# Kernel tuning notes

Measured on AMD Instinct MI355X. Metric: run time of the kernel, lower is better.

The kernel has to match this reference:

```python
import jax, jax.numpy as jnp
import numpy as np

N_NODES = 50000
N_HEDGES = 10000
NNZ_INC = 400000
NNZ_E = 80000
NNZ_V = 400000
VDIM = 128
EDIM = 128
OUT_VDIM = 128
OUT_EDIM = 128


def _spmm(rows, cols, vals, X, n_rows):
    # sparse COO [n_rows, n_cols] @ X  -> [n_rows, d]
    return jax.ops.segment_sum(vals[:, None] * X[cols], rows, num_segments=n_rows)


def setup_inputs() -> dict:
    key = jax.random.key(0)
    ks = jax.random.split(key, 20)
    inp = {
        "vfeat": jax.random.normal(ks[0], (N_NODES, VDIM), jnp.float32),
        "efeat": jax.random.normal(ks[1], (N_HEDGES, EDIM), jnp.float32),
        "invDV": jax.random.uniform(ks[2], (N_NODES,), jnp.float32),
        "invDE": jax.random.uniform(ks[3], (N_HEDGES,), jnp.float32),
        "inc_src": jax.random.randint(ks[4], (NNZ_INC,), 0, N_NODES, jnp.int32),
        "inc_dst": jax.random.randint(ks[5], (NNZ_INC,), 0, N_HEDGES, jnp.int32),
        "emat_rows": jax.random.randint(ks[6], (NNZ_E,), 0, N_HEDGES, jnp.int32),
        "emat_cols": jax.random.randint(ks[7], (NNZ_E,), 0, N_HEDGES, jnp.int32),
        "emat_vals": jax.random.normal(ks[8], (NNZ_E,), jnp.float32),
        "vmat_rows": jax.random.randint(ks[9], (NNZ_V,), 0, N_NODES, jnp.int32),
        "vmat_cols": jax.random.randint(ks[10], (NNZ_V,), 0, N_NODES, jnp.int32),
        "vmat_vals": jax.random.normal(ks[11], (NNZ_V,), jnp.float32),
        # parameters (torch Linear: y = x @ W.T + b)
        "Wv": jax.random.normal(ks[12], (OUT_VDIM, VDIM), jnp.float32) * 0.05,
        "We": jax.random.normal(ks[13], (OUT_EDIM, EDIM), jnp.float32) * 0.05,
        "psi1_W": jax.random.normal(ks[14], (VDIM, VDIM + EDIM), jnp.float32) * 0.05,
        "psi1_b": jnp.zeros((VDIM,), jnp.float32),
        "psi2_W": jax.random.normal(ks[15], (EDIM, OUT_VDIM + EDIM), jnp.float32) * 0.05,
        "psi2_b": jnp.zeros((EDIM,), jnp.float32),
    }
    return inp


def reference(vfeat, efeat, invDV, invDE, inc_src, inc_dst,
              emat_rows, emat_cols, emat_vals,
              vmat_rows, vmat_cols, vmat_vals,
              Wv, We, psi1_W, psi1_b, psi2_W, psi2_b):
    N = vfeat.shape[0]
    E = efeat.shape[0]
    # --- 'in' update_all with psi1: per-incidence concat -> linear -> *invDV[src] -> sum into hyperedge
    x = jnp.concatenate([vfeat[inc_src], efeat[inc_dst]], axis=1)  # [nnz, VDIM+EDIM]
    x = x @ psi1_W.T + psi1_b                                       # [nnz, VDIM]
    x = x * invDV[inc_src][:, None]
    A = jax.ops.segment_sum(x, inc_dst, num_segments=E)             # [E, VDIM]
    A = _spmm(emat_rows, emat_cols, emat_vals, A, E)
    _efeat = A + efeat
    # --- 'con' update_all: node gathers sum of incident hyperedge feats
    _vfeat = jax.ops.segment_sum(_efeat[inc_dst], inc_src, num_segments=N)
    vfeat_out = jax.nn.relu(_vfeat @ Wv.T)                           # [N, OUT_VDIM]
    # --- 'in' update_all with psi2 (dv = ones)
    x2 = jnp.concatenate([vfeat_out[inc_src], efeat[inc_dst]], axis=1)
    x2 = x2 @ psi2_W.T + psi2_b                                      # [nnz, EDIM]
    B = jax.ops.segment_sum(x2, inc_dst, num_segments=E) * invDE[:, None]
    # --- 'con' pass with efeat, then vMat spmm, then 'in' sum back to hyperedges
    _vfeat2 = jax.ops.segment_sum(efeat[inc_dst], inc_src, num_segments=N)
    _vfeat2 = _spmm(vmat_rows, vmat_cols, vmat_vals, _vfeat2, N)
    _efeat2 = jax.ops.segment_sum(_vfeat2[inc_src], inc_dst, num_segments=E)
    _efeat2 = _efeat2 + B
    efeat_out = jax.nn.relu(_efeat2 @ We.T)                          # [E, OUT_EDIM]
    return vfeat_out, efeat_out
```

## Files before the change

kernel.cpp:

```cpp
#include <hip/hip_runtime.h>

#define NN 50000
#define NE 10000
#define NNZ_INC 400000
#define NNZ_E 80000
#define NNZ_V 400000
#define D 128
#define KC 32

#define CAP_D 112
#define CAP_S 40
#define CAP_E 40
#define CAP_V 40

#define GN_ 782
#define GE_ 157
#define G_HINC ((NNZ_INC + 255) / 256)
#define G_EV ((NNZ_E + NNZ_V + 255) / 256)
#define G_CVTN 6250
#define G_CVTE 1250
#define G_NR16 (NN / 16)
#define G_ER16 (NE / 16)

typedef unsigned short u16;
typedef unsigned int u32;

__device__ __forceinline__ u16 f2bf(float x) {
    unsigned u = __float_as_uint(x);
    unsigned r = u + 0x7fffu + ((u >> 16) & 1u);
    return (u16)(r >> 16);
}
__device__ __forceinline__ float bf2f(u16 h) {
    return __uint_as_float(((unsigned)h) << 16);
}

__device__ __forceinline__ void acc8(uint4 u, float acc[8]) {
    acc[0] += __uint_as_float(u.x << 16);
    acc[1] += __uint_as_float(u.x & 0xffff0000u);
    acc[2] += __uint_as_float(u.y << 16);
    acc[3] += __uint_as_float(u.y & 0xffff0000u);
    acc[4] += __uint_as_float(u.z << 16);
    acc[5] += __uint_as_float(u.z & 0xffff0000u);
    acc[6] += __uint_as_float(u.w << 16);
    acc[7] += __uint_as_float(u.w & 0xffff0000u);
}
__device__ __forceinline__ void fma8(uint4 u, float v, float acc[8]) {
    acc[0] = fmaf(v, __uint_as_float(u.x << 16), acc[0]);
    acc[1] = fmaf(v, __uint_as_float(u.x & 0xffff0000u), acc[1]);
    acc[2] = fmaf(v, __uint_as_float(u.y << 16), acc[2]);
    acc[3] = fmaf(v, __uint_as_float(u.y & 0xffff0000u), acc[3]);
    acc[4] = fmaf(v, __uint_as_float(u.z << 16), acc[4]);
    acc[5] = fmaf(v, __uint_as_float(u.z & 0xffff0000u), acc[5]);
    acc[6] = fmaf(v, __uint_as_float(u.w << 16), acc[6]);
    acc[7] = fmaf(v, __uint_as_float(u.w & 0xffff0000u), acc[7]);
}
__device__ __forceinline__ uint4 pack_bf8(const float acc[8]) {
    uint4 o;
    o.x = (u32)f2bf(acc[0]) | ((u32)f2bf(acc[1]) << 16);
    o.y = (u32)f2bf(acc[2]) | ((u32)f2bf(acc[3]) << 16);
    o.z = (u32)f2bf(acc[4]) | ((u32)f2bf(acc[5]) << 16);
    o.w = (u32)f2bf(acc[6]) | ((u32)f2bf(acc[7]) << 16);
    return o;
}

__device__ __forceinline__ void gemm_acc(
    int bx, const float* __restrict__ X, const float* __restrict__ W, int ldw,
    int M, float acc[8][4])
{
    __shared__ float XsT[KC][68];
    __shared__ float Ws[KC][132];
    const int tid = threadIdx.x;
    const int tx = tid & 31, ty = tid >> 5;
    const int row0 = bx * 64;
    const int c0 = tx * 4;
    const int r0 = ty * 8;

#pragma unroll
    for (int r = 0; r < 8; ++r)
#pragma unroll
        for (int c = 0; c < 4; ++c) acc[r][c] = 0.f;

    for (int kc = 0; kc < D; kc += KC) {
        __syncthreads();
#pragma unroll
        for (int it = 0; it < 2; ++it) {
            int l = tid + it * 256;
            int r = l >> 3, k4 = l & 7;
            float4 v = make_float4(0.f, 0.f, 0.f, 0.f);
            int row = row0 + r;
            if (row < M) v = ((const float4*)(X + (size_t)row * D + kc))[k4];
            int k = k4 * 4;
            XsT[k + 0][r] = v.x; XsT[k + 1][r] = v.y;
            XsT[k + 2][r] = v.z; XsT[k + 3][r] = v.w;
        }
#pragma unroll
        for (int it = 0; it < 4; ++it) {
            int l = tid + it * 256;
            int o = l >> 3, k4 = l & 7;
            float4 w = ((const float4*)(W + (size_t)o * ldw + kc))[k4];
            int k = k4 * 4;
            Ws[k + 0][o] = w.x; Ws[k + 1][o] = w.y;
            Ws[k + 2][o] = w.z; Ws[k + 3][o] = w.w;
        }
        __syncthreads();
#pragma unroll
        for (int k = 0; k < KC; ++k) {
            const float4 a0 = *(const float4*)&XsT[k][r0];
            const float4 a1 = *(const float4*)&XsT[k][r0 + 4];
            const float4 b  = *(const float4*)&Ws[k][c0];
            float av[8] = {a0.x, a0.y, a0.z, a0.w, a1.x, a1.y, a1.z, a1.w};
            float bv[4] = {b.x, b.y, b.z, b.w};
#pragma unroll
            for (int r = 0; r < 8; ++r)
#pragma unroll
                for (int c = 0; c < 4; ++c)
                    acc[r][c] = fmaf(av[r], bv[c], acc[r][c]);
        }
    }
}

__global__ __launch_bounds__(256) void mega0(
    const int* __restrict__ inc_src, const int* __restrict__ inc_dst,
    int* __restrict__ cnt_dst, int* __restrict__ cnt_src,
    u16* __restrict__ ell_d, u16* __restrict__ ell_s,
    const float* __restrict__ efeat, const float* __restrict__ vfeat,
    const float* __restrict__ invDV,
    u16* __restrict__ vfi_b, u16* __restrict__ efeat_b)
{
    int b = blockIdx.x;
    if (b < G_HINC) {
        int i = b * 256 + threadIdx.x;
        if (i < NNZ_INC) {
            int s = inc_src[i], d = inc_dst[i];
            int rd = atomicAdd(cnt_dst + d, 1);
            if (rd < CAP_D) ell_d[d * CAP_D + rd] = (u16)s;
            int rs = atomicAdd(cnt_src + s, 1);
            if (rs < CAP_S) ell_s[s * CAP_S + rs] = (u16)d;
        }
    } else if (b < G_HINC + G_CVTN) {
        int i = ((b - G_HINC) * 256 + threadIdx.x) * 4;
        int row = i >> 7;
        float s = invDV[row];
        float4 v = *(const float4*)(vfeat + i);
        ushort4 u;
        u.x = f2bf(v.x * s); u.y = f2bf(v.y * s);
        u.z = f2bf(v.z * s); u.w = f2bf(v.w * s);
        *(ushort4*)(vfi_b + i) = u;
    } else {
        int i = ((b - G_HINC - G_CVTN) * 256 + threadIdx.x) * 4;
        float4 v = *(const float4*)(efeat + i);
        ushort4 u;
        u.x = f2bf(v.x); u.y = f2bf(v.y); u.z = f2bf(v.z); u.w = f2bf(v.w);
        *(ushort4*)(efeat_b + i) = u;
    }
}

__device__ __forceinline__ void segsum_bf_ell16(int rb,
    const int* __restrict__ cnt, int cap, const u16* __restrict__ ell,
    const u16* __restrict__ Tb, u16* __restrict__ Yb, int R)
{
    int r = rb * 16 + (threadIdx.x >> 4);
    int q = threadIdx.x & 15;
    if (r >= R) return;
    int m = min(cnt[r], cap);
    const u16* lst = ell + (size_t)r * cap;
    float acc[8] = {0.f, 0.f, 0.f, 0.f, 0.f, 0.f, 0.f, 0.f};
    int j = 0;
    for (; j + 3 < m; j += 4) {
        ushort4 ix = *(const ushort4*)(lst + j);
        uint4 u0 = *(const uint4*)(Tb + (size_t)ix.x * D + q * 8);
        uint4 u1 = *(const uint4*)(Tb + (size_t)ix.y * D + q * 8);
        uint4 u2 = *(const uint4*)(Tb + (size_t)ix.z * D + q * 8);
        uint4 u3 = *(const uint4*)(Tb + (size_t)ix.w * D + q * 8);
        acc8(u0, acc); acc8(u1, acc); acc8(u2, acc); acc8(u3, acc);
    }
    for (; j < m; ++j) {
        uint4 u0 = *(const uint4*)(Tb + (size_t)lst[j] * D + q * 8);
        acc8(u0, acc);
    }
    ((uint4*)(Yb + (size_t)r * D))[q] = pack_bf8(acc);
}

__device__ __forceinline__ void segsum_f_ell16(int rb,
    const int* __restrict__ cnt, int cap, const u16* __restrict__ ell,
    const u16* __restrict__ Tb, float* __restrict__ Y, int R)
{
    int r = rb * 16 + (threadIdx.x >> 4);
    int q = threadIdx.x & 15;
    if (r >= R) return;
    int m = min(cnt[r], cap);
    const u16* lst = ell + (size_t)r * cap;
    float acc[8] = {0.f, 0.f, 0.f, 0.f, 0.f, 0.f, 0.f, 0.f};
    int j = 0;
    for (; j + 3 < m; j += 4) {
        ushort4 ix = *(const ushort4*)(lst + j);
        uint4 u0 = *(const uint4*)(Tb + (size_t)ix.x * D + q * 8);
        uint4 u1 = *(const uint4*)(Tb + (size_t)ix.y * D + q * 8);
        uint4 u2 = *(const uint4*)(Tb + (size_t)ix.z * D + q * 8);
        uint4 u3 = *(const uint4*)(Tb + (size_t)ix.w * D + q * 8);
        acc8(u0, acc); acc8(u1, acc); acc8(u2, acc); acc8(u3, acc);
    }
    for (; j < m; ++j) {
        uint4 u0 = *(const uint4*)(Tb + (size_t)lst[j] * D + q * 8);
        acc8(u0, acc);
    }
    float* yr = Y + (size_t)r * D;
    ((float4*)yr)[2 * q + 0] = make_float4(acc[0], acc[1], acc[2], acc[3]);
    ((float4*)yr)[2 * q + 1] = make_float4(acc[4], acc[5], acc[6], acc[7]);
}

__device__ __forceinline__ void spmm_bf_ell16(int rb,
    const int* __restrict__ cnt, int cap, const u32* __restrict__ ell,
    const u16* __restrict__ Xb, const float* __restrict__ addend,
    u16* __restrict__ Yb, int R)
{
    int r = rb * 16 + (threadIdx.x >> 4);
    int q = threadIdx.x & 15;
    if (r >= R) return;
    int m = min(cnt[r], cap);
    const u32* lst = ell + (size_t)r * cap;
    float acc[8];
    if (addend) {
        const float* ar = addend + (size_t)r * D;
        float4 lo = ((const float4*)ar)[2 * q + 0];
        float4 hi = ((const float4*)ar)[2 * q + 1];
        acc[0] = lo.x; acc[1] = lo.y; acc[2] = lo.z; acc[3] = lo.w;
        acc[4] = hi.x; acc[5] = hi.y; acc[6] = hi.z; acc[7] = hi.w;
    } else {
#pragma unroll
        for (int i = 0; i < 8; ++i) acc[i] = 0.f;
    }
    int j = 0;
    for (; j + 3 < m; j += 4) {
        uint4 e = *(const uint4*)(lst + j);
        uint4 x0 = *(const uint4*)(Xb + (size_t)(e.x >> 16) * D + q * 8);
        uint4 x1 = *(const uint4*)(Xb + (size_t)(e.y >> 16) * D + q * 8);
        uint4 x2 = *(const uint4*)(Xb + (size_t)(e.z >> 16) * D + q * 8);
        uint4 x3 = *(const uint4*)(Xb + (size_t)(e.w >> 16) * D + q * 8);
        fma8(x0, __uint_as_float(e.x << 16), acc);
        fma8(x1, __uint_as_float(e.y << 16), acc);
        fma8(x2, __uint_as_float(e.z << 16), acc);
        fma8(x3, __uint_as_float(e.w << 16), acc);
    }
    for (; j < m; ++j) {
        u32 e = lst[j];
        uint4 x = *(const uint4*)(Xb + (size_t)(e >> 16) * D + q * 8);
        fma8(x, __uint_as_float(e << 16), acc);
    }
    ((uint4*)(Yb + (size_t)r * D))[q] = pack_bf8(acc);
}

__global__ __launch_bounds__(256) void fusedA(
    const int* __restrict__ erows, const int* __restrict__ ecols,
    const float* __restrict__ evals, int* __restrict__ cnt_e, u32* __restrict__ ev_e,
    const int* __restrict__ vrows, const int* __restrict__ vcols,
    const float* __restrict__ vvals, int* __restrict__ cnt_v, u32* __restrict__ ev_v,
    const float* __restrict__ efeat,
    const float* __restrict__ psi1_W, const float* __restrict__ psi1_b, float* __restrict__ PeP,
    const float* __restrict__ psi2_W, const float* __restrict__ psi2_b, float* __restrict__ QeP,
    const int* __restrict__ cnt_dst, const u16* __restrict__ ell_d,
    const float* __restrict__ invDV, const u16* __restrict__ vfi_b,
    float* __restrict__ sva, float* __restrict__ wsum,
    const int* __restrict__ cnt_src, const u16* __restrict__ ell_s,
    const u16* __restrict__ efeat_b, u16* __restrict__ vf2_b)
{
    int b = blockIdx.x;
    if (b < G_EV) {
        int i = b * 256 + threadIdx.x;
        if (i < NNZ_E) {
            int r = erows[i];
            int re = atomicAdd(cnt_e + r, 1);
            if (re < CAP_E)
                ev_e[r * CAP_E + re] = ((u32)ecols[i] << 16) | (u32)f2bf(evals[i]);
        } else if (i < NNZ_E + NNZ_V) {
            int j = i - NNZ_E;
            int r = vrows[j];
            int rv = atomicAdd(cnt_v + r, 1);
            if (rv < CAP_V)
                ev_v[r * CAP_V + rv] = ((u32)vcols[j] << 16) | (u32)f2bf(vvals[j]);
        }
    } else if (b < G_EV + 2 * GE_) {
        int lb = b - G_EV;
        const float* Wp = (lb < GE_) ? psi1_W + D : psi2_W + D;
        const float* bp = (lb < GE_) ? psi1_b : psi2_b;
        float* outp     = (lb < GE_) ? PeP : QeP;
        int bx = (lb < GE_) ? lb : lb - GE_;
        float acc[8][4];
        gemm_acc(bx, efeat, Wp, 2 * D, NE, acc);
        int tx = threadIdx.x & 31, ty = threadIdx.x >> 5;
        float4 b4 = ((const float4*)bp)[tx];
#pragma unroll
        for (int r = 0; r < 8; ++r) {
            int row = bx * 64 + ty * 8 + r;
            if (row < NE) {
                float4 v = make_float4(acc[r][0] + b4.x, acc[r][1] + b4.y,
                                       acc[r][2] + b4.z, acc[r][3] + b4.w);
                ((float4*)(outp + (size_t)row * D))[tx] = v;
            }
        }
    } else if (b < G_EV + 2 * GE_ + G_ER16) {
        int e = (b - G_EV - 2 * GE_) * 16 + (threadIdx.x >> 4);
        int q = threadIdx.x & 15;
        if (e >= NE) return;
        int m = min(cnt_dst[e], CAP_D);
        const u16* lst = ell_d + (size_t)e * CAP_D;
        float acc[8] = {0.f, 0.f, 0.f, 0.f, 0.f, 0.f, 0.f, 0.f};
        float ws = 0.f;
        int j = 0;
        for (; j + 3 < m; j += 4) {
            ushort4 ix = *(const ushort4*)(lst + j);
            uint4 u0 = *(const uint4*)(vfi_b + (size_t)ix.x * D + q * 8);
            uint4 u1 = *(const uint4*)(vfi_b + (size_t)ix.y * D + q * 8);
            uint4 u2 = *(const uint4*)(vfi_b + (size_t)ix.z * D + q * 8);
            uint4 u3 = *(const uint4*)(vfi_b + (size_t)ix.w * D + q * 8);
            ws += (invDV[ix.x] + invDV[ix.y]) + (invDV[ix.z] + invDV[ix.w]);
            acc8(u0, acc); acc8(u1, acc); acc8(u2, acc); acc8(u3, acc);
        }
        for (; j < m; ++j) {
            int s = lst[j];
            uint4 u0 = *(const uint4*)(vfi_b + (size_t)s * D + q * 8);
            ws += invDV[s];
            acc8(u0, acc);
        }
        float* yr = sva + (size_t)e * D;
        ((float4*)yr)[2 * q + 0] = make_float4(acc[0], acc[1], acc[2], acc[3]);
        ((float4*)yr)[2 * q + 1] = make_float4(acc[4], acc[5], acc[6], acc[7]);
        if (q == 0) wsum[e] = ws;
    } else {
        segsum_bf_ell16(b - G_EV - 2 * GE_ - G_ER16, cnt_src, CAP_S, ell_s, efeat_b, vf2_b, NN);
    }
}

__global__ __launch_bounds__(256) void gemmA_k(
    const float* __restrict__ sva, const float* __restrict__ psi1_W,
    const float* __restrict__ wsum, const float* __restrict__ PeP,
    u16* __restrict__ A_b)
{
    float acc[8][4];
    gemm_acc(blockIdx.x, sva, psi1_W, 2 * D, NE, acc);
    int tx = threadIdx.x & 31, ty = threadIdx.x >> 5;
#pragma unroll
    for (int r = 0; r < 8; ++r) {
        int row = blockIdx.x * 64 + ty * 8 + r;
        if (row < NE) {
            float ws = wsum[row];
            float4 pe = ((const float4*)(PeP + (size_t)row * D))[tx];
            ushort4 u;
            u.x = f2bf(fmaf(ws, pe.x, acc[r][0]));
            u.y = f2bf(fmaf(ws, pe.y, acc[r][1]));
            u.z = f2bf(fmaf(ws, pe.z, acc[r][2]));
            u.w = f2bf(fmaf(ws, pe.w, acc[r][3]));
            ((ushort4*)(A_b + (size_t)row * D))[tx] = u;
        }
    }
}

__global__ __launch_bounds__(256) void fusedB(
    const int* __restrict__ cnt_e, const u32* __restrict__ ev_e,
    const u16* __restrict__ A_b, const float* __restrict__ efeat, u16* __restrict__ A2_b,
    const int* __restrict__ cnt_v, const u32* __restrict__ ev_v,
    const u16* __restrict__ vf2_b, u16* __restrict__ vf2b_b)
{
    int b = blockIdx.x;
    if (b < G_ER16) spmm_bf_ell16(b, cnt_e, CAP_E, ev_e, A_b, efeat, A2_b, NE);
    else spmm_bf_ell16(b - G_ER16, cnt_v, CAP_V, ev_v, vf2_b, nullptr, vf2b_b, NN);
}

__global__ __launch_bounds__(256) void fusedD(
    const int* __restrict__ cnt_src, const u16* __restrict__ ell_s,
    const u16* __restrict__ A2_b, float* __restrict__ vf1,
    const int* __restrict__ cnt_dst, const u16* __restrict__ ell_d,
    const u16* __restrict__ vf2b_b, float* __restrict__ av)
{
    int b = blockIdx.x;
    if (b < G_NR16) segsum_f_ell16(b, cnt_src, CAP_S, ell_s, A2_b, vf1, NN);
    else segsum_f_ell16(b - G_NR16, cnt_dst, CAP_D, ell_d, vf2b_b, av, NE);
}

__global__ __launch_bounds__(256) void gemmC_k(
    const float* __restrict__ vf1, const float* __restrict__ Wv,
    float* __restrict__ out_v, u16* __restrict__ outv_b)
{
    float acc[8][4];
    gemm_acc(blockIdx.x, vf1, Wv, D, NN, acc);
    int tx = threadIdx.x & 31, ty = threadIdx.x >> 5;
#pragma unroll
    for (int r = 0; r < 8; ++r) {
        int row = blockIdx.x * 64 + ty * 8 + r;
        if (row < NN) {
            float4 v = make_float4(fmaxf(acc[r][0], 0.f), fmaxf(acc[r][1], 0.f),
                                   fmaxf(acc[r][2], 0.f), fmaxf(acc[r][3], 0.f));
            ((float4*)(out_v + (size_t)row * D))[tx] = v;
            ushort4 u;
            u.x = f2bf(v.x); u.y = f2bf(v.y); u.z = f2bf(v.z); u.w = f2bf(v.w);
            ((ushort4*)(outv_b + (size_t)row * D))[tx] = u;
        }
    }
}

__global__ __launch_bounds__(256) void gather_sv(
    const int* __restrict__ cnt_dst, const u16* __restrict__ ell_d,
    const u16* __restrict__ outv_b, float* __restrict__ sv)
{
    segsum_f_ell16(blockIdx.x, cnt_dst, CAP_D, ell_d, outv_b, sv, NE);
}

__global__ __launch_bounds__(256) void gemmBE_k(
    const float* __restrict__ sv, const float* __restrict__ psi2_W,
    const int* __restrict__ cnt_dst, const float* __restrict__ QeP,
    const float* __restrict__ invDE, const float* __restrict__ av,
    const float* __restrict__ We, float* __restrict__ out_e)
{
    __shared__ float T[D][68];
    float acc[8][4];
    gemm_acc(blockIdx.x, sv, psi2_W, 2 * D, NE, acc);
    const int tx = threadIdx.x & 31, ty = threadIdx.x >> 5;
    const int bx = blockIdx.x;
#pragma unroll
    for (int r = 0; r < 8; ++r) {
        int row = bx * 64 + ty * 8 + r;
        float deg = 0.f, ide = 0.f;
        float4 qe = make_float4(0.f, 0.f, 0.f, 0.f);
        float4 a  = make_float4(0.f, 0.f, 0.f, 0.f);
        if (row < NE) {
            deg = (float)cnt_dst[row];
            ide = invDE[row];
            qe = ((const float4*)(QeP + (size_t)row * D))[tx];
            a  = ((const float4*)(av  + (size_t)row * D))[tx];
        }
        int lr = ty * 8 + r;
        T[tx * 4 + 0][lr] = fmaf(deg, qe.x, acc[r][0]) * ide + a.x;
        T[tx * 4 + 1][lr] = fmaf(deg, qe.y, acc[r][1]) * ide + a.y;
        T[tx * 4 + 2][lr] = fmaf(deg, qe.z, acc[r][2]) * ide + a.z;
        T[tx * 4 + 3][lr] = fmaf(deg, qe.w, acc[r][3]) * ide + a.w;
    }
    __shared__ float Ws2[KC][132];
    float acc2[8][4];
#pragma unroll
    for (int r = 0; r < 8; ++r)
#pragma unroll
        for (int c = 0; c < 4; ++c) acc2[r][c] = 0.f;
    const int c0 = tx * 4, r0 = ty * 8;
    for (int kc = 0; kc < D; kc += KC) {
        __syncthreads();
#pragma unroll
        for (int it = 0; it < 4; ++it) {
            int l = threadIdx.x + it * 256;
            int o = l >> 3, k4 = l & 7;
            float4 w = ((const float4*)(We + (size_t)o * D + kc))[k4];
            int k = k4 * 4;
            Ws2[k + 0][o] = w.x; Ws2[k + 1][o] = w.y;
            Ws2[k + 2][o] = w.z; Ws2[k + 3][o] = w.w;
        }
        __syncthreads();
#pragma unroll
        for (int k = 0; k < KC; ++k) {
            const float4 a0 = *(const float4*)&T[kc + k][r0];
            const float4 a1 = *(const float4*)&T[kc + k][r0 + 4];
            const float4 bb = *(const float4*)&Ws2[k][c0];
            float avv[8] = {a0.x, a0.y, a0.z, a0.w, a1.x, a1.y, a1.z, a1.w};
            float bv[4] = {bb.x, bb.y, bb.z, bb.w};
#pragma unroll
            for (int r = 0; r < 8; ++r)
#pragma unroll
                for (int c = 0; c < 4; ++c)
                    acc2[r][c] = fmaf(avv[r], bv[c], acc2[r][c]);
        }
    }
#pragma unroll
    for (int r = 0; r < 8; ++r) {
        int row = bx * 64 + ty * 8 + r;
        if (row < NE) {
            float4 v = make_float4(fmaxf(acc2[r][0], 0.f), fmaxf(acc2[r][1], 0.f),
                                   fmaxf(acc2[r][2], 0.f), fmaxf(acc2[r][3], 0.f));
            ((float4*)(out_e + (size_t)row * D))[tx] = v;
        }
    }
}

extern "C" void kernel_launch(void* const* d_in, const int* in_sizes, int n_in,
                              void* d_out, int out_size, void* d_ws, size_t ws_size,
                              hipStream_t stream)
{
    (void)in_sizes; (void)n_in; (void)out_size; (void)ws_size;
    const float* vfeat     = (const float*)d_in[0];
    const float* efeat     = (const float*)d_in[1];
    const float* invDV     = (const float*)d_in[2];
    const float* invDE     = (const float*)d_in[3];
    const int*   inc_src   = (const int*)d_in[4];
    const int*   inc_dst   = (const int*)d_in[5];
    const int*   emat_rows = (const int*)d_in[6];
    const int*   emat_cols = (const int*)d_in[7];
    const float* emat_vals = (const float*)d_in[8];
    const int*   vmat_rows = (const int*)d_in[9];
    const int*   vmat_cols = (const int*)d_in[10];
    const float* vmat_vals = (const float*)d_in[11];
    const float* Wv        = (const float*)d_in[12];
    const float* We        = (const float*)d_in[13];
    const float* psi1_W    = (const float*)d_in[14];
    const float* psi1_b    = (const float*)d_in[15];
    const float* psi2_W    = (const float*)d_in[16];
    const float* psi2_b    = (const float*)d_in[17];

    const size_t ND = (size_t)NN * D;
    const size_t ED = (size_t)NE * D;

    char* p = (char*)d_ws;
    auto alloc = [&](size_t bytes) {
        size_t a = (size_t)p; a = (a + 255) & ~(size_t)255;
        p = (char*)a; void* r = (void*)p; p += bytes; return r;
    };
    float* PeP   = (float*)alloc(ED * 4);
    float* QeP   = (float*)alloc(ED * 4);
    float* vf1   = (float*)alloc(ND * 4);
    float* av    = (float*)alloc(ED * 4);
    float* svbuf = (float*)alloc(ED * 4);
    float* wsum  = (float*)alloc((size_t)NE * 4);
    u16* vfi_b   = (u16*)alloc(ND * 2);
    u16* outv_b  = (u16*)alloc(ND * 2);
    u16* vf2_b   = (u16*)alloc(ND * 2);
    u16* vf2b_b  = (u16*)alloc(ND * 2);
    u16* efeat_b = (u16*)alloc(ED * 2);
    u16* A_b     = (u16*)alloc(ED * 2);
    u16* A2_b    = (u16*)alloc(ED * 2);
    int* cnt_dst = (int*)alloc((size_t)(2 * NE + 2 * NN) * 4);
    int* cnt_src = cnt_dst + NE;
    int* cnt_e   = cnt_src + NN;
    int* cnt_v   = cnt_e + NE;
    u16* ell_d   = (u16*)alloc((size_t)NE * CAP_D * 2);
    u16* ell_s   = (u16*)alloc((size_t)NN * CAP_S * 2);
    u32* ev_e    = (u32*)alloc((size_t)NE * CAP_E * 4);
    u32* ev_v    = (u32*)alloc((size_t)NN * CAP_V * 4);

    float* out_v = (float*)d_out;
    float* out_e = out_v + ND;

    dim3 b256(256);

    hipMemsetAsync(cnt_dst, 0, (size_t)(2 * NE + 2 * NN) * sizeof(int), stream);
    mega0<<<G_HINC + G_CVTN + G_CVTE, b256, 0, stream>>>(
        inc_src, inc_dst, cnt_dst, cnt_src, ell_d, ell_s,
        efeat, vfeat, invDV, vfi_b, efeat_b);
    fusedA<<<G_EV + 2 * GE_ + G_ER16 + G_NR16, b256, 0, stream>>>(
        emat_rows, emat_cols, emat_vals, cnt_e, ev_e,
        vmat_rows, vmat_cols, vmat_vals, cnt_v, ev_v,
        efeat, psi1_W, psi1_b, PeP, psi2_W, psi2_b, QeP,
        cnt_dst, ell_d, invDV, vfi_b, svbuf, wsum,
        cnt_src, ell_s, efeat_b, vf2_b);
    gemmA_k<<<GE_, b256, 0, stream>>>(svbuf, psi1_W, wsum, PeP, A_b);
    fusedB<<<G_ER16 + G_NR16, b256, 0, stream>>>(
        cnt_e, ev_e, A_b, efeat, A2_b,
        cnt_v, ev_v, vf2_b, vf2b_b);
    fusedD<<<G_NR16 + G_ER16, b256, 0, stream>>>(
        cnt_src, ell_s, A2_b, vf1,
        cnt_dst, ell_d, vf2b_b, av);
    gemmC_k<<<GN_, b256, 0, stream>>>(vf1, Wv, out_v, outv_b);
    gather_sv<<<G_ER16, b256, 0, stream>>>(cnt_dst, ell_d, outv_b, svbuf);
    gemmBE_k<<<GE_, b256, 0, stream>>>(svbuf, psi2_W, cnt_dst, QeP, invDE, av, We, out_e);
}
```

Measured before the change: 365.1 us.

## Fold efeat projections into K=256 GEMMs and merge dst-side gathers

Removes the separate PeP/QeP precompute GEMMs from fusedA. It folds the efeat half of psi1/psi2 into gemmA_k and gemmBE_k as a concatenated K=256 GEMM, with the efeat rows scaled by wsum or degree while loading. It also moves the av gather out of fusedD into a new kernel that gathers av and sv in one pass over ell_d. This saves two fp32 ExE buffers and their round trips plus one extra walk of the index list, but the two small serial GEMM kernels now do twice the K work on the critical path.

```diff
diff --git a/kernel.cpp b/kernel.cpp
--- a/kernel.cpp
+++ b/kernel.cpp
@@ -98,6 +98,72 @@
             int l = tid + it * 256;
             int o = l >> 3, k4 = l & 7;
             float4 w = ((const float4*)(W + (size_t)o * ldw + kc))[k4];
+            int k = k4 * 4;
+            Ws[k + 0][o] = w.x; Ws[k + 1][o] = w.y;
+            Ws[k + 2][o] = w.z; Ws[k + 3][o] = w.w;
+        }
+        __syncthreads();
+#pragma unroll
+        for (int k = 0; k < KC; ++k) {
+            const float4 a0 = *(const float4*)&XsT[k][r0];
+            const float4 a1 = *(const float4*)&XsT[k][r0 + 4];
+            const float4 b  = *(const float4*)&Ws[k][c0];
+            float av[8] = {a0.x, a0.y, a0.z, a0.w, a1.x, a1.y, a1.z, a1.w};
+            float bv[4] = {b.x, b.y, b.z, b.w};
+#pragma unroll
+            for (int r = 0; r < 8; ++r)
+#pragma unroll
+                for (int c = 0; c < 4; ++c)
+                    acc[r][c] = fmaf(av[r], bv[c], acc[r][c]);
+        }
+    }
+}
+
+__device__ __forceinline__ void gemm_acc2(
+    int bx, const float* __restrict__ X1, const float* __restrict__ X2,
+    const float* __restrict__ rsf, const int* __restrict__ rsi,
+    const float* __restrict__ W, int M, float acc[8][4])
+{
+    __shared__ float XsT[KC][68];
+    __shared__ float Ws[KC][132];
+    const int tid = threadIdx.x;
+    const int tx = tid & 31, ty = tid >> 5;
+    const int row0 = bx * 64;
+    const int c0 = tx * 4;
+    const int r0 = ty * 8;
+
+#pragma unroll
+    for (int r = 0; r < 8; ++r)
+#pragma unroll
+        for (int c = 0; c < 4; ++c) acc[r][c] = 0.f;
+
+    for (int kc = 0; kc < 2 * D; kc += KC) {
+        __syncthreads();
+        const bool second = (kc >= D);
+        const float* Xp = second ? X2 : X1;
+        const int kk = second ? kc - D : kc;
+#pragma unroll
+        for (int it = 0; it < 2; ++it) {
+            int l = tid + it * 256;
+            int r = l >> 3, k4 = l & 7;
+            float4 v = make_float4(0.f, 0.f, 0.f, 0.f);
+            int row = row0 + r;
+            if (row < M) {
+                v = ((const float4*)(Xp + (size_t)row * D + kk))[k4];
+                if (second) {
+                    float sc = rsf ? rsf[row] : (float)rsi[row];
+                    v.x *= sc; v.y *= sc; v.z *= sc; v.w *= sc;
+                }
+            }
+            int k = k4 * 4;
+            XsT[k + 0][r] = v.x; XsT[k + 1][r] = v.y;
+            XsT[k + 2][r] = v.z; XsT[k + 3][r] = v.w;
+        }
+#pragma unroll
+        for (int it = 0; it < 4; ++it) {
+            int l = tid + it * 256;
+            int o = l >> 3, k4 = l & 7;
+            float4 w = ((const float4*)(W + (size_t)o * (2 * D) + kc))[k4];
             int k = k4 * 4;
             Ws[k + 0][o] = w.x; Ws[k + 1][o] = w.y;
             Ws[k + 2][o] = w.z; Ws[k + 3][o] = w.w;
@@ -255,9 +321,6 @@
     const float* __restrict__ evals, int* __restrict__ cnt_e, u32* __restrict__ ev_e,
     const int* __restrict__ vrows, const int* __restrict__ vcols,
     const float* __restrict__ vvals, int* __restrict__ cnt_v, u32* __restrict__ ev_v,
-    const float* __restrict__ efeat,
-    const float* __restrict__ psi1_W, const float* __restrict__ psi1_b, float* __restrict__ PeP,
-    const float* __restrict__ psi2_W, const float* __restrict__ psi2_b, float* __restrict__ QeP,
     const int* __restrict__ cnt_dst, const u16* __restrict__ ell_d,
     const float* __restrict__ invDV, const u16* __restrict__ vfi_b,
     float* __restrict__ sva, float* __restrict__ wsum,
@@ -279,27 +342,8 @@
             if (rv < CAP_V)
                 ev_v[r * CAP_V + rv] = ((u32)vcols[j] << 16) | (u32)f2bf(vvals[j]);
         }
-    } else if (b < G_EV + 2 * GE_) {
-        int lb = b - G_EV;
-        const float* Wp = (lb < GE_) ? psi1_W + D : psi2_W + D;
-        const float* bp = (lb < GE_) ? psi1_b : psi2_b;
-        float* outp     = (lb < GE_) ? PeP : QeP;
-        int bx = (lb < GE_) ? lb : lb - GE_;
-        float acc[8][4];
-        gemm_acc(bx, efeat, Wp, 2 * D, NE, acc);
-        int tx = threadIdx.x & 31, ty = threadIdx.x >> 5;
-        float4 b4 = ((const float4*)bp)[tx];
-#pragma unroll
-        for (int r = 0; r < 8; ++r) {
-            int row = bx * 64 + ty * 8 + r;
-            if (row < NE) {
-                float4 v = make_float4(acc[r][0] + b4.x, acc[r][1] + b4.y,
-                                       acc[r][2] + b4.z, acc[r][3] + b4.w);
-                ((float4*)(outp + (size_t)row * D))[tx] = v;
-            }
-        }
-    } else if (b < G_EV + 2 * GE_ + G_ER16) {
-        int e = (b - G_EV - 2 * GE_) * 16 + (threadIdx.x >> 4);
+    } else if (b < G_EV + G_ER16) {
+        int e = (b - G_EV) * 16 + (threadIdx.x >> 4);
         int q = threadIdx.x & 15;
         if (e >= NE) return;
         int m = min(cnt_dst[e], CAP_D);
@@ -327,29 +371,30 @@
         ((float4*)yr)[2 * q + 1] = make_float4(acc[4], acc[5], acc[6], acc[7]);
         if (q == 0) wsum[e] = ws;
     } else {
-        segsum_bf_ell16(b - G_EV - 2 * GE_ - G_ER16, cnt_src, CAP_S, ell_s, efeat_b, vf2_b, NN);
+        segsum_bf_ell16(b - G_EV - G_ER16, cnt_src, CAP_S, ell_s, efeat_b, vf2_b, NN);
     }
 }
 
 __global__ __launch_bounds__(256) void gemmA_k(
-    const float* __restrict__ sva, const float* __restrict__ psi1_W,
-    const float* __restrict__ wsum, const float* __restrict__ PeP,
+    const float* __restrict__ sva, const float* __restrict__ efeat,
+    const float* __restrict__ wsum,
+    const float* __restrict__ psi1_W, const float* __restrict__ psi1_b,
     u16* __restrict__ A_b)
 {
     float acc[8][4];
-    gemm_acc(blockIdx.x, sva, psi1_W, 2 * D, NE, acc);
+    gemm_acc2(blockIdx.x, sva, efeat, wsum, nullptr, psi1_W, NE, acc);
     int tx = threadIdx.x & 31, ty = threadIdx.x >> 5;
+    float4 b4 = ((const float4*)psi1_b)[tx];
 #pragma unroll
     for (int r = 0; r < 8; ++r) {
         int row = blockIdx.x * 64 + ty * 8 + r;
         if (row < NE) {
             float ws = wsum[row];
-            float4 pe = ((const float4*)(PeP + (size_t)row * D))[tx];
             ushort4 u;
-            u.x = f2bf(fmaf(ws, pe.x, acc[r][0]));
-            u.y = f2bf(fmaf(ws, pe.y, acc[r][1]));
-            u.z = f2bf(fmaf(ws, pe.z, acc[r][2]));
-            u.w = f2bf(fmaf(ws, pe.w, acc[r][3]));
+            u.x = f2bf(fmaf(ws, b4.x, acc[r][0]));
+            u.y = f2bf(fmaf(ws, b4.y, acc[r][1]));
+            u.z = f2bf(fmaf(ws, b4.z, acc[r][2]));
+            u.w = f2bf(fmaf(ws, b4.w, acc[r][3]));
             ((ushort4*)(A_b + (size_t)row * D))[tx] = u;
         }
     }
@@ -368,13 +413,9 @@
 
 __global__ __launch_bounds__(256) void fusedD(
     const int* __restrict__ cnt_src, const u16* __restrict__ ell_s,
-    const u16* __restrict__ A2_b, float* __restrict__ vf1,
-    const int* __restrict__ cnt_dst, const u16* __restrict__ ell_d,
-    const u16* __restrict__ vf2b_b, float* __restrict__ av)
-{
-    int b = blockIdx.x;
-    if (b < G_NR16) segsum_f_ell16(b, cnt_src, CAP_S, ell_s, A2_b, vf1, NN);
-    else segsum_f_ell16(b - G_NR16, cnt_dst, CAP_D, ell_d, vf2b_b, av, NE);
+    const u16* __restrict__ A2_b, float* __restrict__ vf1)
+{
+    segsum_f_ell16(blockIdx.x, cnt_src, CAP_S, ell_s, A2_b, vf1, NN);
 }
 
 __global__ __launch_bounds__(256) void gemmC_k(
@@ -398,41 +439,70 @@
     }
 }
 
-__global__ __launch_bounds__(256) void gather_sv(
+__global__ __launch_bounds__(256) void gather_avsv(
     const int* __restrict__ cnt_dst, const u16* __restrict__ ell_d,
-    const u16* __restrict__ outv_b, float* __restrict__ sv)
-{
-    segsum_f_ell16(blockIdx.x, cnt_dst, CAP_D, ell_d, outv_b, sv, NE);
+    const u16* __restrict__ vf2b_b, const u16* __restrict__ outv_b,
+    float* __restrict__ av, float* __restrict__ sv)
+{
+    int r = blockIdx.x * 16 + (threadIdx.x >> 4);
+    int q = threadIdx.x & 15;
+    if (r >= NE) return;
+    int m = min(cnt_dst[r], CAP_D);
+    const u16* lst = ell_d + (size_t)r * CAP_D;
+    float a[8] = {0.f, 0.f, 0.f, 0.f, 0.f, 0.f, 0.f, 0.f};
+    float s[8] = {0.f, 0.f, 0.f, 0.f, 0.f, 0.f, 0.f, 0.f};
+    int j = 0;
+    for (; j + 1 < m; j += 2) {
+        ushort2 ix = *(const ushort2*)(lst + j);
+        uint4 a0 = *(const uint4*)(vf2b_b + (size_t)ix.x * D + q * 8);
+        uint4 a1 = *(const uint4*)(vf2b_b + (size_t)ix.y * D + q * 8);
+        uint4 s0 = *(const uint4*)(outv_b + (size_t)ix.x * D + q * 8);
+        uint4 s1 = *(const uint4*)(outv_b + (size_t)ix.y * D + q * 8);
+        acc8(a0, a); acc8(a1, a);
+        acc8(s0, s); acc8(s1, s);
+    }
+    for (; j < m; ++j) {
+        int ix = lst[j];
+        uint4 a0 = *(const uint4*)(vf2b_b + (size_t)ix * D + q * 8);
+        uint4 s0 = *(const uint4*)(outv_b + (size_t)ix * D + q * 8);
+        acc8(a0, a); acc8(s0, s);
+    }
+    float* ar = av + (size_t)r * D;
+    ((float4*)ar)[2 * q + 0] = make_float4(a[0], a[1], a[2], a[3]);
+    ((float4*)ar)[2 * q + 1] = make_float4(a[4], a[5], a[6], a[7]);
+    float* sr = sv + (size_t)r * D;
+    ((float4*)sr)[2 * q + 0] = make_float4(s[0], s[1], s[2], s[3]);
+    ((float4*)sr)[2 * q + 1] = make_float4(s[4], s[5], s[6], s[7]);
 }
 
 __global__ __launch_bounds__(256) void gemmBE_k(
-    const float* __restrict__ sv, const float* __restrict__ psi2_W,
-    const int* __restrict__ cnt_dst, const float* __restrict__ QeP,
+    const float* __restrict__ sv, const float* __restrict__ efeat,
+    const int* __restrict__ cnt_dst,
+    const float* __restrict__ psi2_W, const float* __restrict__ psi2_b,
     const float* __restrict__ invDE, const float* __restrict__ av,
     const float* __restrict__ We, float* __restrict__ out_e)
 {
     __shared__ float T[D][68];
     float acc[8][4];
-    gemm_acc(blockIdx.x, sv, psi2_W, 2 * D, NE, acc);
+    gemm_acc2(blockIdx.x, sv, efeat, nullptr, cnt_dst, psi2_W, NE, acc);
     const int tx = threadIdx.x & 31, ty = threadIdx.x >> 5;
     const int bx = blockIdx.x;
+    float4 b2 = ((const float4*)psi2_b)[tx];
 #pragma unroll
     for (int r = 0; r < 8; ++r) {
         int row = bx * 64 + ty * 8 + r;
         float deg = 0.f, ide = 0.f;
-        float4 qe = make_float4(0.f, 0.f, 0.f, 0.f);
-        float4 a  = make_float4(0.f, 0.f, 0.f, 0.f);
+        float4 a = make_float4(0.f, 0.f, 0.f, 0.f);
         if (row < NE) {
             deg = (float)cnt_dst[row];
             ide = invDE[row];
-            qe = ((const float4*)(QeP + (size_t)row * D))[tx];
-            a  = ((const float4*)(av  + (size_t)row * D))[tx];
+            a = ((const float4*)(av + (size_t)row * D))[tx];
         }
         int lr = ty * 8 + r;
-        T[tx * 4 + 0][lr] = fmaf(deg, qe.x, acc[r][0]) * ide + a.x;
-        T[tx * 4 + 1][lr] = fmaf(deg, qe.y, acc[r][1]) * ide + a.y;
-        T[tx * 4 + 2][lr] = fmaf(deg, qe.z, acc[r][2]) * ide + a.z;
-        T[tx * 4 + 3][lr] = fmaf(deg, qe.w, acc[r][3]) * ide + a.w;
+        T[tx * 4 + 0][lr] = fmaf(deg, b2.x, acc[r][0]) * ide + a.x;
+        T[tx * 4 + 1][lr] = fmaf(deg, b2.y, acc[r][1]) * ide + a.y;
+        T[tx * 4 + 2][lr] = fmaf(deg, b2.z, acc[r][2]) * ide + a.z;
+        T[tx * 4 + 3][lr] = fmaf(deg, b2.w, acc[r][3]) * ide + a.w;
     }
     __shared__ float Ws2[KC][132];
     float acc2[8][4];
@@ -510,8 +580,6 @@
         size_t a = (size_t)p; a = (a + 255) & ~(size_t)255;
         p = (char*)a; void* r = (void*)p; p += bytes; return r;
     };
-    float* PeP   = (float*)alloc(ED * 4);
-    float* QeP   = (float*)alloc(ED * 4);
     float* vf1   = (float*)alloc(ND * 4);
     float* av    = (float*)alloc(ED * 4);
     float* svbuf = (float*)alloc(ED * 4);
@@ -541,20 +609,19 @@
     mega0<<<G_HINC + G_CVTN + G_CVTE, b256, 0, stream>>>(
         inc_src, inc_dst, cnt_dst, cnt_src, ell_d, ell_s,
         efeat, vfeat, invDV, vfi_b, efeat_b);
-    fusedA<<<G_EV + 2 * GE_ + G_ER16 + G_NR16, b256, 0, stream>>>(
+    fusedA<<<G_EV + G_ER16 + G_NR16, b256, 0, stream>>>(
         emat_rows, emat_cols, emat_vals, cnt_e, ev_e,
         vmat_rows, vmat_cols, vmat_vals, cnt_v, ev_v,
-        efeat, psi1_W, psi1_b, PeP, psi2_W, psi2_b, QeP,
         cnt_dst, ell_d, invDV, vfi_b, svbuf, wsum,
         cnt_src, ell_s, efeat_b, vf2_b);
-    gemmA_k<<<GE_, b256, 0, stream>>>(svbuf, psi1_W, wsum, PeP, A_b);
+    gemmA_k<<<GE_, b256, 0, stream>>>(svbuf, efeat, wsum, psi1_W, psi1_b, A_b);
     fusedB<<<G_ER16 + G_NR16, b256, 0, stream>>>(
         cnt_e, ev_e, A_b, efeat, A2_b,
         cnt_v, ev_v, vf2_b, vf2b_b);
-    fusedD<<<G_NR16 + G_ER16, b256, 0, stream>>>(
-        cnt_src, ell_s, A2_b, vf1,
-        cnt_dst, ell_d, vf2b_b, av);
+    fusedD<<<G_NR16, b256, 0, stream>>>(cnt_src, ell_s, A2_b, vf1);
     gemmC_k<<<GN_, b256, 0, stream>>>(vf1, Wv, out_v, outv_b);
-    gather_sv<<<G_ER16, b256, 0, stream>>>(cnt_dst, ell_d, outv_b, svbuf);
-    gemmBE_k<<<GE_, b256, 0, stream>>>(svbuf, psi2_W, cnt_dst, QeP, invDE, av, We, out_e);
-}
+    gather_avsv<<<G_ER16, b256, 0, stream>>>(
+        cnt_dst, ell_d, vf2b_b, outv_b, av, svbuf);
+    gemmBE_k<<<GE_, b256, 0, stream>>>(
+        svbuf, efeat, cnt_dst, psi2_W, psi2_b, invDE, av, We, out_e);
+}
```

After: 387.1 us. +6.0%, slower.
